# Performance work log

Measured on AMD Instinct MI355X. Metric: run time of the kernel, lower is better.

## Reference

```python
import jax, jax.numpy as jnp
import numpy as np
import math

NHEAD = 8
NEG = -1e9  # stand-in for float('-inf') in the torch mask

def _layernorm(x, g, b):
    m = x.mean(-1, keepdims=True)
    v = ((x - m) ** 2).mean(-1, keepdims=True)
    return (x - m) / jnp.sqrt(v + 1e-5) * g + b

def setup_inputs() -> dict:
    key = jax.random.key(0)
    ks = jax.random.split(key, 8)
    B, S, D, E, F, L, C = 32, 512, 9, 256, 1024, 4, 10
    p = lambda k, shape: jax.random.normal(k, shape, dtype=jnp.float32) * 0.02
    return dict(
        src=jax.random.normal(ks[0], (B, S, D), dtype=jnp.float32),
        emb_W=p(ks[1], (E, D)), emb_b=jnp.zeros((E,), jnp.float32),
        Wqkv=p(ks[2], (L, 3 * E, E)), bqkv=jnp.zeros((L, 3 * E), jnp.float32),
        Wo=p(ks[3], (L, E, E)), bo=jnp.zeros((L, E), jnp.float32),
        ln1_g=jnp.ones((L, E), jnp.float32), ln1_b=jnp.zeros((L, E), jnp.float32),
        ln2_g=jnp.ones((L, E), jnp.float32), ln2_b=jnp.zeros((L, E), jnp.float32),
        W1=p(ks[4], (L, F, E)), b1=jnp.zeros((L, F), jnp.float32),
        W2=p(ks[5], (L, E, F)), b2=jnp.zeros((L, E), jnp.float32),
        dec_W=p(ks[6], (C, E)),
    )

def reference(src, emb_W, emb_b, Wqkv, bqkv, Wo, bo, ln1_g, ln1_b,
              ln2_g, ln2_b, W1, b1, W2, b2, dec_W):
    B, S, _ = src.shape
    E = emb_W.shape[0]
    H = NHEAD
    hd = E // H
    L = Wqkv.shape[0]

    # custom sparse mask: diagonal-only attention, except the last query row
    # attends to everything but itself (has_src_mask=True branch)
    eye = jnp.eye(S, dtype=src.dtype)
    mask = jnp.where(eye > 0, 0.0, NEG)
    mask = mask.at[-1, :].set(0.0).at[-1, -1].set(NEG)

    # sinusoidal positional encoding [S, E]
    pos = jnp.arange(S, dtype=jnp.float32)[:, None]
    div = jnp.exp(jnp.arange(0, E, 2, dtype=jnp.float32) * (-math.log(10000.0) / E))
    pe = jnp.zeros((S, E), jnp.float32)
    pe = pe.at[:, 0::2].set(jnp.sin(pos * div)).at[:, 1::2].set(jnp.cos(pos * div))

    # embed + scale + pos-enc (batch-first layout; math identical to seq-first)
    x = (src @ emb_W.T + emb_b) * math.sqrt(E) + pe[None, :, :]

    attns = []
    for l in range(L):  # small fixed number of layers
        qkv = x @ Wqkv[l].T + bqkv[l]  # [B,S,3E]
        q, k, v = jnp.split(qkv, 3, axis=-1)
        rs = lambda t: t.reshape(B, S, H, hd).transpose(0, 2, 1, 3)  # [B,H,S,hd]
        q, k, v = rs(q), rs(k), rs(v)
        scores = jnp.einsum('bhqd,bhkd->bhqk', q, k) / math.sqrt(hd) + mask
        a = jax.nn.softmax(scores, axis=-1)
        attns.append(a.mean(axis=1))  # head-averaged attention, as torch MHA returns
        o = jnp.einsum('bhqk,bhkd->bhqd', a, v).transpose(0, 2, 1, 3).reshape(B, S, E)
        x = _layernorm(x + (o @ Wo[l].T + bo[l]), ln1_g[l], ln1_b[l])
        f = jax.nn.relu(x @ W1[l].T + b1[l]) @ W2[l].T + b2[l]
        x = _layernorm(x + f, ln2_g[l], ln2_b[l])

    x = jax.nn.relu(x)
    out = (x @ dec_W.T).mean(axis=1)  # mean over sequence
    out = jax.nn.log_softmax(out, axis=-1)
    return out, jnp.stack(attns)
```

## Files before the change

### kernel.cpp

```cpp
#include <hip/hip_runtime.h>
#include <hip/hip_bf16.h>
#include <math.h>

namespace {

constexpr int BATCH = 32;
constexpr int SEQ   = 512;
constexpr int DIN   = 9;
constexpr int EMB   = 256;
constexpr int FF    = 1024;
constexpr int NLAYER= 4;
constexpr int NCLS  = 10;
constexpr int NHEADS= 8;
constexpr int HDIM  = 32;
constexpr int NTOK  = BATCH*SEQ;

typedef __attribute__((ext_vector_type(8))) short short8;
typedef __attribute__((ext_vector_type(4))) float floatx4;

#define GLOAD_LDS16(g, l) __builtin_amdgcn_global_load_lds( \
    (const __attribute__((address_space(1))) unsigned*)(g), \
    (__attribute__((address_space(3))) unsigned*)(l), 16, 0, 0)

#define WAITCNT(N) asm volatile("s_waitcnt vmcnt(" #N ")" ::: "memory")

template<bool RELU, bool KV>
__global__ __launch_bounds__(256)
void gemm_mfma(const __hip_bfloat16* __restrict__ A, int lda,
               const __hip_bfloat16* __restrict__ W,
               const float* __restrict__ bias,
               __hip_bfloat16* __restrict__ C0,
               __hip_bfloat16* __restrict__ C1,
               int ldc, int K)
{
    __shared__ __hip_bfloat16 As[2*128*32];
    __shared__ __hip_bfloat16 Bs[2*128*32];
    const int bm = blockIdx.y*128, bn = blockIdx.x*128;
    const int tid  = threadIdx.x;
    const int lane = tid & 63;
    const int w    = tid >> 6;
    const int wm   = (w >> 1)*64, wn = (w & 1)*64;

    floatx4 acc[4][4] = {};

    const int srow = w*32 + (lane >> 2);
    const int scol = (lane & 3)*8;
    const __hip_bfloat16* gA0 = A + (size_t)(bm + srow)*lda + scol;
    const __hip_bfloat16* gA1 = A + (size_t)(bm + srow + 16)*lda + scol;
    const __hip_bfloat16* gB0 = W + (size_t)(bn + srow)*K + scol;
    const __hip_bfloat16* gB1 = W + (size_t)(bn + srow + 16)*K + scol;
    const int l0 = (w*2)*512, l1 = (w*2 + 1)*512;

#define GM_STAGE(buf, k0) do { \
    GLOAD_LDS16(gA0 + (k0), As + (buf)*4096 + l0); \
    GLOAD_LDS16(gA1 + (k0), As + (buf)*4096 + l1); \
    GLOAD_LDS16(gB0 + (k0), Bs + (buf)*4096 + l0); \
    GLOAD_LDS16(gB1 + (k0), Bs + (buf)*4096 + l1); } while (0)

    const int arow = wm + (lane & 15);
    const int brow = wn + (lane & 15);
    const int kh   = lane >> 4;
    const int nt   = K >> 5;

    GM_STAGE(0, 0);
    for (int t = 0; t < nt; t++) {
        const int cur = t & 1;
        if (t + 1 < nt) {
            GM_STAGE(cur ^ 1, (t+1)*32);
            WAITCNT(4);
        } else {
            WAITCNT(0);
        }
        __builtin_amdgcn_s_barrier();
        const short8* Ab = (const short8*)(As + cur*4096);
        const short8* Bb = (const short8*)(Bs + cur*4096);
        short8 af[4], bf[4];
        #pragma unroll
        for (int m = 0; m < 4; m++) af[m] = Ab[(arow + m*16)*4 + kh];
        #pragma unroll
        for (int n = 0; n < 4; n++) bf[n] = Bb[(brow + n*16)*4 + kh];
        #pragma unroll
        for (int m = 0; m < 4; m++)
            #pragma unroll
            for (int n = 0; n < 4; n++)
                acc[m][n] = __builtin_amdgcn_mfma_f32_16x16x32_bf16(af[m], bf[n], acc[m][n], 0, 0, 0);
        __builtin_amdgcn_s_barrier();
    }
#undef GM_STAGE

    __hip_bfloat16* Cb;
    int cb;
    if (KV && bn >= 256) { Cb = C1; cb = bn - 256; }
    else                 { Cb = C0; cb = bn; }

    const int crow0 = bm + wm + (lane >> 4)*4;
    #pragma unroll
    for (int n = 0; n < 4; n++) {
        const int coln = wn + (lane & 15) + n*16;
        const float bv = bias[bn + coln];
        #pragma unroll
        for (int m = 0; m < 4; m++) {
            #pragma unroll
            for (int r = 0; r < 4; r++) {
                int row = crow0 + m*16 + r;
                float v = acc[m][n][r] + bv;
                if (RELU) v = fmaxf(v, 0.f);
                Cb[(size_t)row*ldc + cb + coln] = __float2bfloat16(v);
            }
        }
    }
}

__device__ __forceinline__ void stageB64(const __hip_bfloat16* __restrict__ W, int ldw,
                                         int rowbase, int kbase,
                                         __hip_bfloat16* LB, int buf, int w, int lane)
{
    #pragma unroll
    for (int i = 0; i < 2; i++) {
        int rc = 2*w + i;
        const __hip_bfloat16* src = W + (size_t)(rowbase + rc*16 + (lane >> 2))*ldw
                                      + kbase + (lane & 3)*8;
        GLOAD_LDS16(src, LB + buf*8192 + rc*512);
    }
}

__device__ __forceinline__ void mfma8(const short8* Ab, const short8* Bb,
                                      floatx4* acc, int rgrp, int colhalf,
                                      int cl, int kh)
{
    short8 af = Ab[rgrp*64 + cl*4 + kh];
    #pragma unroll
    for (int n = 0; n < 8; n++) {
        short8 bf = Bb[(colhalf*8 + n)*64 + cl*4 + kh];
        acc[n] = __builtin_amdgcn_mfma_f32_16x16x32_bf16(af, bf, acc[n], 0, 0, 0);
    }
}

__global__ __launch_bounds__(512, 2)
void layer_tail(const __hip_bfloat16* __restrict__ vbuf,
                const __hip_bfloat16* __restrict__ obuf,
                const __hip_bfloat16* __restrict__ Wo,
                const float* __restrict__ bo,
                const float* __restrict__ g1, const float* __restrict__ b1ln,
                const __hip_bfloat16* __restrict__ W1,
                const float* __restrict__ b1f,
                const __hip_bfloat16* __restrict__ W2,
                const float* __restrict__ b2f,
                const float* __restrict__ g2, const float* __restrict__ b2ln,
                __hip_bfloat16* __restrict__ xb16,
                const __hip_bfloat16* __restrict__ Wkv,
                const float* __restrict__ bk,
                const float* __restrict__ bv2,
                __hip_bfloat16* __restrict__ kout,
                __hip_bfloat16* __restrict__ vout)
{
    __shared__ __hip_bfloat16 SM[63488];
    __hip_bfloat16* LB = SM;
    __hip_bfloat16* LA = SM + 24576;
    __hip_bfloat16* X1 = SM + 30720;
    __hip_bfloat16* HC = SM + 47104;
    float* RED = (float*)LA;

    const int bm   = blockIdx.x*64;
    const int tid  = threadIdx.x;
    const int lane = tid & 63;
    const int w    = tid >> 6;
    const int rgrp = w & 3;
    const int colhalf = w >> 2;
    const int cl   = lane & 15;
    const int rg   = lane >> 4;
    const int kh   = rg;

    floatx4 acc[8] = {};
    const __hip_bfloat16* asrc = nullptr;
    if (w >= 4) {
        int a = w - 4;
        int grow = bm + a*16 + (lane >> 2);
        bool isl = (grow & (SEQ-1)) == (SEQ-1);
        asrc = (isl ? obuf + (size_t)(grow >> 9)*EMB
                    : vbuf + (size_t)grow*EMB) + (lane & 3)*8;
    }
    stageB64(Wo, 256, 0, 0, LB, 0, w, lane);
    if (w >= 4) GLOAD_LDS16(asrc, LA + (w-4)*512);
    stageB64(Wo, 256, 0, 32, LB, 1, w, lane);
    if (w >= 4) GLOAD_LDS16(asrc + 32, LA + 2048 + (w-4)*512);
    for (int t = 0; t < 8; t++) {
        const int cur = t % 3;
        if (t + 2 < 8) {
            const int nb = (t+2) % 3;
            stageB64(Wo, 256, 0, (t+2)*32, LB, nb, w, lane);
            if (w >= 4) GLOAD_LDS16(asrc + (t+2)*32, LA + nb*2048 + (w-4)*512);
        }
        if (w >= 4) { if (t < 6) WAITCNT(6); else if (t == 6) WAITCNT(3); else WAITCNT(0); }
        else        { if (t < 6) WAITCNT(4); else if (t == 6) WAITCNT(2); else WAITCNT(0); }
        __builtin_amdgcn_s_barrier();
        mfma8((const short8*)(LA + cur*2048), (const short8*)(LB + cur*8192),
              acc, rgrp, colhalf, cl, kh);
        __builtin_amdgcn_s_barrier();
    }
    {
        float gv[8], bbv[8], bv[8];
        #pragma unroll
        for (int n = 0; n < 8; n++) {
            int col = colhalf*128 + n*16 + cl;
            bv[n] = bo[col]; gv[n] = g1[col]; bbv[n] = b1ln[col];
        }
        #pragma unroll
        for (int r = 0; r < 4; r++) {
            int row = bm + rgrp*16 + rg*4 + r;
            const __hip_bfloat16* xr = xb16 + (size_t)row*EMB + colhalf*128;
            float S = 0.f, Q = 0.f;
            #pragma unroll
            for (int n = 0; n < 8; n++) {
                float v = acc[n][r] + bv[n] + __bfloat162float(xr[n*16 + cl]);
                acc[n][r] = v; S += v; Q += v*v;
            }
            #pragma unroll
            for (int o = 1; o < 16; o <<= 1) { S += __shfl_xor(S, o); Q += __shfl_xor(Q, o); }
            if (cl == 0) {
                int idx = rgrp*16 + rg*4 + r;
                RED[colhalf*64 + idx] = S;
                RED[128 + colhalf*64 + idx] = Q;
            }
        }
        __syncthreads();
        #pragma unroll
        for (int r = 0; r < 4; r++) {
            int idx = rgrp*16 + rg*4 + r;
            float S = RED[idx] + RED[64 + idx];
            float Q = RED[128 + idx] + RED[192 + idx];
            float mean = S * (1.f/EMB);
            float var  = Q * (1.f/EMB) - mean*mean;
            float rstd = 1.f / sqrtf(var + 1e-5f);
            #pragma unroll
            for (int n = 0; n < 8; n++) {
                int col = colhalf*128 + n*16 + cl;
                float v = (acc[n][r] - mean)*rstd*gv[n] + bbv[n];
                X1[(col >> 5)*2048 + rgrp*512 + (rg*4 + r)*32 + (col & 31)] = __float2bfloat16(v);
            }
        }
        __syncthreads();
    }

    floatx4 acc2[8] = {};
    for (int c = 0; c < 4; c++) {
        floatx4 fa[8] = {};
        stageB64(W1, 256, c*256, 0, LB, 0, w, lane);
        stageB64(W1, 256, c*256, 32, LB, 1, w, lane);
        for (int t = 0; t < 8; t++) {
            const int cur = t % 3;
            if (t + 2 < 8) stageB64(W1, 256, c*256, (t+2)*32, LB, (t+2)%3, w, lane);
            if (t < 6) WAITCNT(4); else if (t == 6) WAITCNT(2); else WAITCNT(0);
            __builtin_amdgcn_s_barrier();
            mfma8((const short8*)X1 + t*256, (const short8*)(LB + cur*8192),
                  fa, rgrp, colhalf, cl, kh);
            __builtin_amdgcn_s_barrier();
        }
        #pragma unroll
        for (int n = 0; n < 8; n++) {
            int colh = colhalf*128 + n*16 + cl;
            float bb = b1f[c*256 + colh];
            #pragma unroll
            for (int r = 0; r < 4; r++) {
                float v = fmaxf(fa[n][r] + bb, 0.f);
                HC[(colh >> 5)*2048 + rgrp*512 + (rg*4 + r)*32 + (colh & 31)] = __float2bfloat16(v);
            }
        }
        __syncthreads();
        stageB64(W2, 1024, 0, c*256, LB, 0, w, lane);
        stageB64(W2, 1024, 0, c*256 + 32, LB, 1, w, lane);
        for (int t = 0; t < 8; t++) {
            const int cur = t % 3;
            if (t + 2 < 8) stageB64(W2, 1024, 0, c*256 + (t+2)*32, LB, (t+2)%3, w, lane);
            if (t < 6) WAITCNT(4); else if (t == 6) WAITCNT(2); else WAITCNT(0);
            __builtin_amdgcn_s_barrier();
            mfma8((const short8*)HC + t*256, (const short8*)(LB + cur*8192),
                  acc2, rgrp, colhalf, cl, kh);
            __builtin_amdgcn_s_barrier();
        }
    }

    {
        float gv[8], bbv[8], bv[8];
        #pragma unroll
        for (int n = 0; n < 8; n++) {
            int col = colhalf*128 + n*16 + cl;
            bv[n] = b2f[col]; gv[n] = g2[col]; bbv[n] = b2ln[col];
        }
        #pragma unroll
        for (int r = 0; r < 4; r++) {
            float S = 0.f, Q = 0.f;
            #pragma unroll
            for (int n = 0; n < 8; n++) {
                int col = colhalf*128 + n*16 + cl;
                float x1v = __bfloat162float(X1[(col >> 5)*2048 + rgrp*512 + (rg*4 + r)*32 + (col & 31)]);
                float v = acc2[n][r] + bv[n] + x1v;
                acc2[n][r] = v; S += v; Q += v*v;
            }
            #pragma unroll
            for (int o = 1; o < 16; o <<= 1) { S += __shfl_xor(S, o); Q += __shfl_xor(Q, o); }
            if (cl == 0) {
                int idx = rgrp*16 + rg*4 + r;
                RED[colhalf*64 + idx] = S;
                RED[128 + colhalf*64 + idx] = Q;
            }
        }
        __syncthreads();
        #pragma unroll
        for (int r = 0; r < 4; r++) {
            int idx = rgrp*16 + rg*4 + r;
            int row = bm + idx;
            float S = RED[idx] + RED[64 + idx];
            float Q = RED[128 + idx] + RED[192 + idx];
            float mean = S * (1.f/EMB);
            float var  = Q * (1.f/EMB) - mean*mean;
            float rstd = 1.f / sqrtf(var + 1e-5f);
            __hip_bfloat16* xr = xb16 + (size_t)row*EMB + colhalf*128;
            #pragma unroll
            for (int n = 0; n < 8; n++) {
                int col = colhalf*128 + n*16 + cl;
                float v = (acc2[n][r] - mean)*rstd*gv[n] + bbv[n];
                __hip_bfloat16 hv = __float2bfloat16(v);
                xr[n*16 + cl] = hv;
                HC[(col >> 5)*2048 + rgrp*512 + (rg*4 + r)*32 + (col & 31)] = hv;
            }
        }
        __syncthreads();
    }

    if (Wkv != nullptr) {
        #pragma unroll
        for (int nh = 0; nh < 2; nh++) {
            floatx4 a3[8] = {};
            const float* bkv = (nh == 0) ? bk : bv2;
            __hip_bfloat16* dst = (nh == 0) ? kout : vout;
            stageB64(Wkv, 256, nh*256, 0, LB, 0, w, lane);
            stageB64(Wkv, 256, nh*256, 32, LB, 1, w, lane);
            for (int t = 0; t < 8; t++) {
                const int cur = t % 3;
                if (t + 2 < 8) stageB64(Wkv, 256, nh*256, (t+2)*32, LB, (t+2)%3, w, lane);
                if (t < 6) WAITCNT(4); else if (t == 6) WAITCNT(2); else WAITCNT(0);
                __builtin_amdgcn_s_barrier();
                mfma8((const short8*)HC + t*256, (const short8*)(LB + cur*8192),
                      a3, rgrp, colhalf, cl, kh);
                __builtin_amdgcn_s_barrier();
            }
            #pragma unroll
            for (int n = 0; n < 8; n++) {
                int col = colhalf*128 + n*16 + cl;
                float bb = bkv[col];
                #pragma unroll
                for (int r = 0; r < 4; r++) {
                    int row = bm + rgrp*16 + rg*4 + r;
                    dst[(size_t)row*EMB + col] = __float2bfloat16(a3[n][r] + bb);
                }
            }
        }
    }
}

__global__ void f2b_all(const float* __restrict__ s0, const float* __restrict__ s1,
                        const float* __restrict__ s2, const float* __restrict__ s3,
                        __hip_bfloat16* __restrict__ d0, __hip_bfloat16* __restrict__ d1,
                        __hip_bfloat16* __restrict__ d2, __hip_bfloat16* __restrict__ d3)
{
    int blk = blockIdx.x;
    const float* s; __hip_bfloat16* d; int base;
    if      (blk <  768) { s = s0; d = d0; base = blk; }
    else if (blk < 1024) { s = s1; d = d1; base = blk - 768; }
    else if (blk < 2048) { s = s2; d = d2; base = blk - 1024; }
    else                 { s = s3; d = d3; base = blk - 2048; }
    int i = (base*256 + threadIdx.x)*4;
    float4 v = *(const float4*)(s + i);
    __hip_bfloat16 tmp[4];
    tmp[0] = __float2bfloat16(v.x); tmp[1] = __float2bfloat16(v.y);
    tmp[2] = __float2bfloat16(v.z); tmp[3] = __float2bfloat16(v.w);
    *(ushort4*)(d + i) = *(const ushort4*)tmp;
}

__global__ void embed_kernel(const float* __restrict__ src,
                             const float* __restrict__ emb_W,
                             const float* __restrict__ emb_b,
                             __hip_bfloat16* __restrict__ xb)
{
    int row = blockIdx.x;
    int e = threadIdx.x;
    int s = row % SEQ;
    const float* sr = src + (size_t)row*DIN;
    float acc = emb_b[e];
    #pragma unroll
    for (int d = 0; d < DIN; d++) acc += sr[d]*emb_W[e*DIN + d];
    acc *= 16.0f;
    int i2 = e & ~1;
    float div = expf(-(float)i2 * (9.210340371976184f / (float)EMB));
    float ang = (float)s * div;
    float pe = (e & 1) ? cosf(ang) : sinf(ang);
    xb[(size_t)row*EMB + e] = __float2bfloat16(acc + pe);
}

__global__ __launch_bounds__(512)
void attn_last_head(const __hip_bfloat16* __restrict__ xb,
                    const __hip_bfloat16* __restrict__ Wq,
                    const float* __restrict__ bq,
                    const __hip_bfloat16* __restrict__ kbuf,
                    const __hip_bfloat16* __restrict__ vbuf,
                    __hip_bfloat16* __restrict__ obuf,
                    float* __restrict__ amh)
{
    const int h = blockIdx.x, b = blockIdx.y;
    const int t = threadIdx.x;
    __shared__ float xlast[EMB];
    __shared__ float qpart[HDIM][17];
    __shared__ float qh[HDIM];
    __shared__ float sc[SEQ];
    __shared__ float red1[8], red2[8];
    __shared__ float opart[16][HDIM];

    if (t < EMB) xlast[t] = __bfloat162float(xb[((size_t)b*SEQ + SEQ-1)*EMB + t]);
    __syncthreads();

    {
        int d = t & 31, c = t >> 5;
        const __hip_bfloat16* wr = Wq + (size_t)(h*HDIM + d)*EMB + c*16;
        short8 w0 = *(const short8*)(wr);
        short8 w1 = *(const short8*)(wr + 8);
        float p = 0.f;
        #pragma unroll
        for (int j = 0; j < 8; j++)
            p += xlast[c*16 + j]*__bfloat162float(((const __hip_bfloat16*)&w0)[j]);
        #pragma unroll
        for (int j = 0; j < 8; j++)
            p += xlast[c*16 + 8 + j]*__bfloat162float(((const __hip_bfloat16*)&w1)[j]);
        qpart[d][c] = p;
    }
    __syncthreads();
    if (t < HDIM) {
        float qv = bq[h*HDIM + t];
        #pragma unroll
        for (int c = 0; c < 16; c++) qv += qpart[t][c];
        qh[t] = qv;
    }
    __syncthreads();

    {
        const __hip_bfloat16* krow = kbuf + ((size_t)b*SEQ + t)*EMB + h*HDIM;
        float s = 0.f;
        #pragma unroll
        for (int vv = 0; vv < 4; vv++) {
            short8 kk = *(const short8*)(krow + vv*8);
            #pragma unroll
            for (int j = 0; j < 8; j++)
                s += qh[vv*8 + j]*__bfloat162float(((const __hip_bfloat16*)&kk)[j]);
        }
        s *= 0.17677669529663687f;
        if (t == SEQ-1) s += -1e9f;
        sc[t] = s;
    }
    __syncthreads();

    {
        int wv = t >> 6, lane = t & 63;
        float m = sc[t];
        #pragma unroll
        for (int o = 32; o; o >>= 1) m = fmaxf(m, __shfl_xor(m, o));
        if (lane == 0) red1[wv] = m;
        __syncthreads();
        m = red1[0];
        #pragma unroll
        for (int i = 1; i < 8; i++) m = fmaxf(m, red1[i]);
        float e = expf(sc[t] - m);
        float s = e;
        #pragma unroll
        for (int o = 32; o; o >>= 1) s += __shfl_xor(s, o);
        if (lane == 0) red2[wv] = s;
        __syncthreads();
        float tot = red2[0]+red2[1]+red2[2]+red2[3]+red2[4]+red2[5]+red2[6]+red2[7];
        float a = e / tot;
        sc[t] = a;
        amh[((size_t)b*NHEADS + h)*SEQ + t] = a;
    }
    __syncthreads();

    {
        int e = t & 31, part = t >> 5;
        float o = 0.f;
        const __hip_bfloat16* vc = vbuf + (size_t)b*SEQ*EMB + h*HDIM + e;
        for (int k = part*32; k < part*32 + 32; k++)
            o += sc[k]*__bfloat162float(vc[(size_t)k*EMB]);
        opart[part][e] = o;
    }
    __syncthreads();
    if (t < HDIM) {
        float o = 0.f;
        #pragma unroll
        for (int p = 0; p < 16; p++) o += opart[p][t];
        obuf[b*EMB + h*HDIM + t] = __float2bfloat16(o);
    }
}

__global__ void write_attns(float* __restrict__ attns, const float* __restrict__ amh_all)
{
    constexpr int PER_ROW = SEQ/4;
    size_t tid = (size_t)blockIdx.x*blockDim.x + threadIdx.x;
    size_t row = tid / PER_ROW;
    int c4 = (int)(tid % PER_ROW);
    int q = (int)(row % SEQ);
    float4 v = make_float4(0.f,0.f,0.f,0.f);
    if (q == SEQ-1) {
        size_t lb = row / SEQ;
        const float* base = amh_all + lb*NHEADS*SEQ + c4*4;
        float x0=0.f, x1=0.f, x2=0.f, x3=0.f;
        #pragma unroll
        for (int h = 0; h < NHEADS; h++) {
            const float* r = base + (size_t)h*SEQ;
            x0 += r[0]; x1 += r[1]; x2 += r[2]; x3 += r[3];
        }
        v = make_float4(x0*0.125f, x1*0.125f, x2*0.125f, x3*0.125f);
    } else if ((q >> 2) == c4) {
        ((float*)&v)[q & 3] = 1.f;
    }
    ((float4*)attns)[tid] = v;
}

__global__ __launch_bounds__(512)
void decode_fused(const __hip_bfloat16* __restrict__ xb, const float* __restrict__ dec_W,
                  float* __restrict__ out)
{
    int b = blockIdx.x, t = threadIdx.x;
    int e = t & 255, half = t >> 8;
    __shared__ float rs[2][256];
    {
        const __hip_bfloat16* xp = xb + ((size_t)b*SEQ + half*256)*EMB + e;
        float r = 0.f;
        for (int i = 0; i < 256; i++) r += fmaxf(__bfloat162float(xp[(size_t)i*EMB]), 0.f);
        rs[half][e] = r;
    }
    __syncthreads();
    float part[NCLS];
    if (t < 256) {
        float rr = rs[0][t] + rs[1][t];
        #pragma unroll
        for (int c = 0; c < NCLS; c++) part[c] = rr * dec_W[c*EMB + t];
    } else {
        #pragma unroll
        for (int c = 0; c < NCLS; c++) part[c] = 0.f;
    }
    #pragma unroll
    for (int o = 32; o; o >>= 1)
        #pragma unroll
        for (int c = 0; c < NCLS; c++) part[c] += __shfl_xor(part[c], o);
    __shared__ float red[8][NCLS];
    int wv = t >> 6, lane = t & 63;
    if (lane == 0)
        #pragma unroll
        for (int c = 0; c < NCLS; c++) red[wv][c] = part[c];
    __syncthreads();
    if (t == 0) {
        float lg[NCLS];
        float m = -1e30f;
        #pragma unroll
        for (int c = 0; c < NCLS; c++) {
            float s = 0.f;
            #pragma unroll
            for (int wvi = 0; wvi < 8; wvi++) s += red[wvi][c];
            lg[c] = s * (1.f/(float)SEQ);
            m = fmaxf(m, lg[c]);
        }
        float s = 0.f;
        #pragma unroll
        for (int c = 0; c < NCLS; c++) s += expf(lg[c] - m);
        float ls = logf(s);
        #pragma unroll
        for (int c = 0; c < NCLS; c++) out[b*NCLS + c] = lg[c] - m - ls;
    }
}

}

extern "C" void kernel_launch(void* const* d_in, const int* in_sizes, int n_in,
                              void* d_out, int out_size, void* d_ws, size_t ws_size,
                              hipStream_t stream)
{
    const float* src   = (const float*)d_in[0];
    const float* emb_W = (const float*)d_in[1];
    const float* emb_b = (const float*)d_in[2];
    const float* Wqkv  = (const float*)d_in[3];
    const float* bqkv  = (const float*)d_in[4];
    const float* Wo    = (const float*)d_in[5];
    const float* bo    = (const float*)d_in[6];
    const float* ln1_g = (const float*)d_in[7];
    const float* ln1_b = (const float*)d_in[8];
    const float* ln2_g = (const float*)d_in[9];
    const float* ln2_b = (const float*)d_in[10];
    const float* W1    = (const float*)d_in[11];
    const float* b1    = (const float*)d_in[12];
    const float* W2    = (const float*)d_in[13];
    const float* b2    = (const float*)d_in[14];
    const float* dec_W = (const float*)d_in[15];

    float* out   = (float*)d_out;
    float* attns = out + BATCH*NCLS;

    char* ws = (char*)d_ws;
    __hip_bfloat16* xb16 = (__hip_bfloat16*)ws;     ws += (size_t)NTOK*EMB*2;
    __hip_bfloat16* kbuf = (__hip_bfloat16*)ws;     ws += (size_t)NTOK*EMB*2;
    __hip_bfloat16* vbuf = (__hip_bfloat16*)ws;     ws += (size_t)NTOK*EMB*2;
    __hip_bfloat16* obuf = (__hip_bfloat16*)ws;     ws += (size_t)BATCH*EMB*2;
    __hip_bfloat16* wq16 = (__hip_bfloat16*)ws;     ws += (size_t)NLAYER*3*EMB*EMB*2;
    __hip_bfloat16* wo16 = (__hip_bfloat16*)ws;     ws += (size_t)NLAYER*EMB*EMB*2;
    __hip_bfloat16* w116 = (__hip_bfloat16*)ws;     ws += (size_t)NLAYER*FF*EMB*2;
    __hip_bfloat16* w216 = (__hip_bfloat16*)ws;     ws += (size_t)NLAYER*EMB*FF*2;
    float*          amall= (float*)ws;              ws += (size_t)NLAYER*BATCH*NHEADS*SEQ*4;

    f2b_all<<<3072, 256, 0, stream>>>(Wqkv, Wo, W1, W2, wq16, wo16, w116, w216);

    embed_kernel<<<NTOK, EMB, 0, stream>>>(src, emb_W, emb_b, xb16);

    gemm_mfma<false, true><<<dim3(512/128, NTOK/128), 256, 0, stream>>>(
        xb16, EMB, wq16 + (size_t)EMB*EMB, bqkv + EMB, kbuf, vbuf, EMB, EMB);

    for (int l = 0; l < NLAYER; l++) {
        const __hip_bfloat16* wql = wq16 + (size_t)l*3*EMB*EMB;
        const float* bql = bqkv + (size_t)l*3*EMB;

        attn_last_head<<<dim3(NHEADS, BATCH), 512, 0, stream>>>(
            xb16, wql, bql, kbuf, vbuf, obuf, amall + (size_t)l*BATCH*NHEADS*SEQ);

        const bool last = (l == NLAYER-1);
        const __hip_bfloat16* wkv_next = last ? nullptr
            : wq16 + (size_t)(l+1)*3*EMB*EMB + (size_t)EMB*EMB;
        const float* bk_next = last ? nullptr : bqkv + (size_t)(l+1)*3*EMB + EMB;
        const float* bv_next = last ? nullptr : bqkv + (size_t)(l+1)*3*EMB + 2*EMB;
        layer_tail<<<NTOK/64, 512, 0, stream>>>(
            vbuf, obuf,
            wo16 + (size_t)l*EMB*EMB, bo + (size_t)l*EMB,
            ln1_g + l*EMB, ln1_b + l*EMB,
            w116 + (size_t)l*FF*EMB, b1 + (size_t)l*FF,
            w216 + (size_t)l*EMB*FF, b2 + (size_t)l*EMB,
            ln2_g + l*EMB, ln2_b + l*EMB,
            xb16,
            wkv_next, bk_next, bv_next,
            last ? nullptr : kbuf, last ? nullptr : vbuf);
    }

    {
        size_t total_f4 = (size_t)NLAYER*BATCH*SEQ*(SEQ/4);
        int blocks = (int)((total_f4 + 255)/256);
        write_attns<<<blocks, 256, 0, stream>>>(attns, amall);
    }

    decode_fused<<<BATCH, 512, 0, stream>>>(xb16, dec_W, out);
}
```

Before: 444.5 us.

## Fuse embedding into K/V projection and use 4-deep buffers without trailing barrier

Replaces the separate embedding kernel and generic GEMM for the first layer's K/V projection with a single kernel. It computes the embedded tile into shared memory and immediately runs the MFMA projection, so the embedding output is never read back from global memory. In layer_tail and the new kernel, the weight staging ring grows from 3 to 4 slots, which lets the second barrier per k-step be dropped. The cost is more LDS per block (about 144KB for layer_tail), which may lower occupancy below the 2 blocks per CU its launch bounds request.

```diff
diff --git a/kernel.cpp b/kernel.cpp
--- a/kernel.cpp
+++ b/kernel.cpp
@@ -23,93 +23,6 @@
     (__attribute__((address_space(3))) unsigned*)(l), 16, 0, 0)
 
 #define WAITCNT(N) asm volatile("s_waitcnt vmcnt(" #N ")" ::: "memory")
-
-template<bool RELU, bool KV>
-__global__ __launch_bounds__(256)
-void gemm_mfma(const __hip_bfloat16* __restrict__ A, int lda,
-               const __hip_bfloat16* __restrict__ W,
-               const float* __restrict__ bias,
-               __hip_bfloat16* __restrict__ C0,
-               __hip_bfloat16* __restrict__ C1,
-               int ldc, int K)
-{
-    __shared__ __hip_bfloat16 As[2*128*32];
-    __shared__ __hip_bfloat16 Bs[2*128*32];
-    const int bm = blockIdx.y*128, bn = blockIdx.x*128;
-    const int tid  = threadIdx.x;
-    const int lane = tid & 63;
-    const int w    = tid >> 6;
-    const int wm   = (w >> 1)*64, wn = (w & 1)*64;
-
-    floatx4 acc[4][4] = {};
-
-    const int srow = w*32 + (lane >> 2);
-    const int scol = (lane & 3)*8;
-    const __hip_bfloat16* gA0 = A + (size_t)(bm + srow)*lda + scol;
-    const __hip_bfloat16* gA1 = A + (size_t)(bm + srow + 16)*lda + scol;
-    const __hip_bfloat16* gB0 = W + (size_t)(bn + srow)*K + scol;
-    const __hip_bfloat16* gB1 = W + (size_t)(bn + srow + 16)*K + scol;
-    const int l0 = (w*2)*512, l1 = (w*2 + 1)*512;
-
-#define GM_STAGE(buf, k0) do { \
-    GLOAD_LDS16(gA0 + (k0), As + (buf)*4096 + l0); \
-    GLOAD_LDS16(gA1 + (k0), As + (buf)*4096 + l1); \
-    GLOAD_LDS16(gB0 + (k0), Bs + (buf)*4096 + l0); \
-    GLOAD_LDS16(gB1 + (k0), Bs + (buf)*4096 + l1); } while (0)
-
-    const int arow = wm + (lane & 15);
-    const int brow = wn + (lane & 15);
-    const int kh   = lane >> 4;
-    const int nt   = K >> 5;
-
-    GM_STAGE(0, 0);
-    for (int t = 0; t < nt; t++) {
-        const int cur = t & 1;
-        if (t + 1 < nt) {
-            GM_STAGE(cur ^ 1, (t+1)*32);
-            WAITCNT(4);
-        } else {
-            WAITCNT(0);
-        }
-        __builtin_amdgcn_s_barrier();
-        const short8* Ab = (const short8*)(As + cur*4096);
-        const short8* Bb = (const short8*)(Bs + cur*4096);
-        short8 af[4], bf[4];
-        #pragma unroll
-        for (int m = 0; m < 4; m++) af[m] = Ab[(arow + m*16)*4 + kh];
-        #pragma unroll
-        for (int n = 0; n < 4; n++) bf[n] = Bb[(brow + n*16)*4 + kh];
-        #pragma unroll
-        for (int m = 0; m < 4; m++)
-            #pragma unroll
-            for (int n = 0; n < 4; n++)
-                acc[m][n] = __builtin_amdgcn_mfma_f32_16x16x32_bf16(af[m], bf[n], acc[m][n], 0, 0, 0);
-        __builtin_amdgcn_s_barrier();
-    }
-#undef GM_STAGE
-
-    __hip_bfloat16* Cb;
-    int cb;
-    if (KV && bn >= 256) { Cb = C1; cb = bn - 256; }
-    else                 { Cb = C0; cb = bn; }
-
-    const int crow0 = bm + wm + (lane >> 4)*4;
-    #pragma unroll
-    for (int n = 0; n < 4; n++) {
-        const int coln = wn + (lane & 15) + n*16;
-        const float bv = bias[bn + coln];
-        #pragma unroll
-        for (int m = 0; m < 4; m++) {
-            #pragma unroll
-            for (int r = 0; r < 4; r++) {
-                int row = crow0 + m*16 + r;
-                float v = acc[m][n][r] + bv;
-                if (RELU) v = fmaxf(v, 0.f);
-                Cb[(size_t)row*ldc + cb + coln] = __float2bfloat16(v);
-            }
-        }
-    }
-}
 
 __device__ __forceinline__ void stageB64(const __hip_bfloat16* __restrict__ W, int ldw,
                                          int rowbase, int kbase,
@@ -154,11 +67,11 @@
                 __hip_bfloat16* __restrict__ kout,
                 __hip_bfloat16* __restrict__ vout)
 {
-    __shared__ __hip_bfloat16 SM[63488];
+    __shared__ __hip_bfloat16 SM[73728];
     __hip_bfloat16* LB = SM;
-    __hip_bfloat16* LA = SM + 24576;
-    __hip_bfloat16* X1 = SM + 30720;
-    __hip_bfloat16* HC = SM + 47104;
+    __hip_bfloat16* LA = SM + 32768;
+    __hip_bfloat16* X1 = SM + 40960;
+    __hip_bfloat16* HC = SM + 57344;
     float* RED = (float*)LA;
 
     const int bm   = blockIdx.x*64;
@@ -185,9 +98,9 @@
     stageB64(Wo, 256, 0, 32, LB, 1, w, lane);
     if (w >= 4) GLOAD_LDS16(asrc + 32, LA + 2048 + (w-4)*512);
     for (int t = 0; t < 8; t++) {
-        const int cur = t % 3;
+        const int cur = t & 3;
         if (t + 2 < 8) {
-            const int nb = (t+2) % 3;
+            const int nb = (t+2) & 3;
             stageB64(Wo, 256, 0, (t+2)*32, LB, nb, w, lane);
             if (w >= 4) GLOAD_LDS16(asrc + (t+2)*32, LA + nb*2048 + (w-4)*512);
         }
@@ -196,7 +109,6 @@
         __builtin_amdgcn_s_barrier();
         mfma8((const short8*)(LA + cur*2048), (const short8*)(LB + cur*8192),
               acc, rgrp, colhalf, cl, kh);
-        __builtin_amdgcn_s_barrier();
     }
     {
         float gv[8], bbv[8], bv[8];
@@ -248,13 +160,12 @@
         stageB64(W1, 256, c*256, 0, LB, 0, w, lane);
         stageB64(W1, 256, c*256, 32, LB, 1, w, lane);
         for (int t = 0; t < 8; t++) {
-            const int cur = t % 3;
-            if (t + 2 < 8) stageB64(W1, 256, c*256, (t+2)*32, LB, (t+2)%3, w, lane);
+            const int cur = t & 3;
+            if (t + 2 < 8) stageB64(W1, 256, c*256, (t+2)*32, LB, (t+2)&3, w, lane);
             if (t < 6) WAITCNT(4); else if (t == 6) WAITCNT(2); else WAITCNT(0);
             __builtin_amdgcn_s_barrier();
             mfma8((const short8*)X1 + t*256, (const short8*)(LB + cur*8192),
                   fa, rgrp, colhalf, cl, kh);
-            __builtin_amdgcn_s_barrier();
         }
         #pragma unroll
         for (int n = 0; n < 8; n++) {
@@ -270,14 +181,14 @@
         stageB64(W2, 1024, 0, c*256, LB, 0, w, lane);
         stageB64(W2, 1024, 0, c*256 + 32, LB, 1, w, lane);
         for (int t = 0; t < 8; t++) {
-            const int cur = t % 3;
-            if (t + 2 < 8) stageB64(W2, 1024, 0, c*256 + (t+2)*32, LB, (t+2)%3, w, lane);
+            const int cur = t & 3;
+            if (t + 2 < 8) stageB64(W2, 1024, 0, c*256 + (t+2)*32, LB, (t+2)&3, w, lane);
             if (t < 6) WAITCNT(4); else if (t == 6) WAITCNT(2); else WAITCNT(0);
             __builtin_amdgcn_s_barrier();
             mfma8((const short8*)HC + t*256, (const short8*)(LB + cur*8192),
                   acc2, rgrp, colhalf, cl, kh);
-            __builtin_amdgcn_s_barrier();
-        }
+        }
+        __syncthreads();
     }
 
     {
@@ -337,13 +248,12 @@
             stageB64(Wkv, 256, nh*256, 0, LB, 0, w, lane);
             stageB64(Wkv, 256, nh*256, 32, LB, 1, w, lane);
             for (int t = 0; t < 8; t++) {
-                const int cur = t % 3;
-                if (t + 2 < 8) stageB64(Wkv, 256, nh*256, (t+2)*32, LB, (t+2)%3, w, lane);
+                const int cur = t & 3;
+                if (t + 2 < 8) stageB64(Wkv, 256, nh*256, (t+2)*32, LB, (t+2)&3, w, lane);
                 if (t < 6) WAITCNT(4); else if (t == 6) WAITCNT(2); else WAITCNT(0);
                 __builtin_amdgcn_s_barrier();
                 mfma8((const short8*)HC + t*256, (const short8*)(LB + cur*8192),
                       a3, rgrp, colhalf, cl, kh);
-                __builtin_amdgcn_s_barrier();
             }
             #pragma unroll
             for (int n = 0; n < 8; n++) {
@@ -354,6 +264,84 @@
                     int row = bm + rgrp*16 + rg*4 + r;
                     dst[(size_t)row*EMB + col] = __float2bfloat16(a3[n][r] + bb);
                 }
+            }
+        }
+    }
+}
+
+__global__ __launch_bounds__(512, 2)
+void embed_kv(const float* __restrict__ src,
+              const float* __restrict__ emb_W,
+              const float* __restrict__ emb_b,
+              const __hip_bfloat16* __restrict__ Wkv,
+              const float* __restrict__ bk,
+              const float* __restrict__ bv2,
+              __hip_bfloat16* __restrict__ xb16,
+              __hip_bfloat16* __restrict__ kout,
+              __hip_bfloat16* __restrict__ vout)
+{
+    __shared__ __hip_bfloat16 SM2[49152];
+    __hip_bfloat16* LB = SM2;
+    __hip_bfloat16* XC = SM2 + 32768;
+
+    const int bm   = blockIdx.x*64;
+    const int tid  = threadIdx.x;
+    const int lane = tid & 63;
+    const int w    = tid >> 6;
+    const int rgrp = w & 3;
+    const int colhalf = w >> 2;
+    const int cl   = lane & 15;
+    const int rg   = lane >> 4;
+    const int kh   = rg;
+
+    stageB64(Wkv, 256, 0, 0, LB, 0, w, lane);
+    stageB64(Wkv, 256, 0, 32, LB, 1, w, lane);
+
+    for (int i = 0; i < 32; i++) {
+        int idx = tid + i*512;
+        int rr = idx >> 8, e = idx & 255;
+        int row = bm + rr;
+        int s = row & (SEQ-1);
+        const float* sr = src + (size_t)row*DIN;
+        float acc = emb_b[e];
+        #pragma unroll
+        for (int d = 0; d < DIN; d++) acc += sr[d]*emb_W[e*DIN + d];
+        acc *= 16.0f;
+        int i2 = e & ~1;
+        float div = expf(-(float)i2 * (9.210340371976184f / (float)EMB));
+        float ang = (float)s * div;
+        float pe = (e & 1) ? cosf(ang) : sinf(ang);
+        __hip_bfloat16 hv = __float2bfloat16(acc + pe);
+        xb16[(size_t)row*EMB + e] = hv;
+        XC[(e >> 5)*2048 + rr*32 + (e & 31)] = hv;
+    }
+    __syncthreads();
+
+    #pragma unroll
+    for (int nh = 0; nh < 2; nh++) {
+        floatx4 a3[8] = {};
+        const float* bkv = (nh == 0) ? bk : bv2;
+        __hip_bfloat16* dst = (nh == 0) ? kout : vout;
+        if (nh == 1) {
+            stageB64(Wkv, 256, 256, 0, LB, 0, w, lane);
+            stageB64(Wkv, 256, 256, 32, LB, 1, w, lane);
+        }
+        for (int t = 0; t < 8; t++) {
+            const int cur = t & 3;
+            if (t + 2 < 8) stageB64(Wkv, 256, nh*256, (t+2)*32, LB, (t+2)&3, w, lane);
+            if (t < 6) WAITCNT(4); else if (t == 6) WAITCNT(2); else WAITCNT(0);
+            __builtin_amdgcn_s_barrier();
+            mfma8((const short8*)XC + t*256, (const short8*)(LB + cur*8192),
+                  a3, rgrp, colhalf, cl, kh);
+        }
+        #pragma unroll
+        for (int n = 0; n < 8; n++) {
+            int col = colhalf*128 + n*16 + cl;
+            float bb = bkv[col];
+            #pragma unroll
+            for (int r = 0; r < 4; r++) {
+                int row = bm + rgrp*16 + rg*4 + r;
+                dst[(size_t)row*EMB + col] = __float2bfloat16(a3[n][r] + bb);
             }
         }
     }
@@ -376,26 +364,6 @@
     tmp[0] = __float2bfloat16(v.x); tmp[1] = __float2bfloat16(v.y);
     tmp[2] = __float2bfloat16(v.z); tmp[3] = __float2bfloat16(v.w);
     *(ushort4*)(d + i) = *(const ushort4*)tmp;
-}
-
-__global__ void embed_kernel(const float* __restrict__ src,
-                             const float* __restrict__ emb_W,
-                             const float* __restrict__ emb_b,
-                             __hip_bfloat16* __restrict__ xb)
-{
-    int row = blockIdx.x;
-    int e = threadIdx.x;
-    int s = row % SEQ;
-    const float* sr = src + (size_t)row*DIN;
-    float acc = emb_b[e];
-    #pragma unroll
-    for (int d = 0; d < DIN; d++) acc += sr[d]*emb_W[e*DIN + d];
-    acc *= 16.0f;
-    int i2 = e & ~1;
-    float div = expf(-(float)i2 * (9.210340371976184f / (float)EMB));
-    float ang = (float)s * div;
-    float pe = (e & 1) ? cosf(ang) : sinf(ang);
-    xb[(size_t)row*EMB + e] = __float2bfloat16(acc + pe);
 }
 
 __global__ __launch_bounds__(512)
@@ -614,10 +582,10 @@
 
     f2b_all<<<3072, 256, 0, stream>>>(Wqkv, Wo, W1, W2, wq16, wo16, w116, w216);
 
-    embed_kernel<<<NTOK, EMB, 0, stream>>>(src, emb_W, emb_b, xb16);
-
-    gemm_mfma<false, true><<<dim3(512/128, NTOK/128), 256, 0, stream>>>(
-        xb16, EMB, wq16 + (size_t)EMB*EMB, bqkv + EMB, kbuf, vbuf, EMB, EMB);
+    embed_kv<<<NTOK/64, 512, 0, stream>>>(
+        src, emb_W, emb_b,
+        wq16 + (size_t)EMB*EMB, bqkv + EMB, bqkv + 2*EMB,
+        xb16, kbuf, vbuf);
 
     for (int l = 0; l < NLAYER; l++) {
         const __hip_bfloat16* wql = wq16 + (size_t)l*3*EMB*EMB;
```

Measured after the change: 442.1 us. No clear change (-0.5%).
